# Kernel tuning notes

Measured on AMD Instinct MI355X. Metric: run time of the kernel, lower is better.

The kernel has to match this reference:

```python
import jax, jax.numpy as jnp
import numpy as np

V, F = 100000, 200000
N, H, W, K = 4, 512, 512, 4
SIGMA = 1e-4
GAMMA = 1e-4
BG = (1.0, 1.0, 1.0)
EPS = 1e-10
ZNEAR, ZFAR = 1.0, 100.0


def setup_inputs() -> dict:
    key = jax.random.key(0)
    ks = jax.random.split(key, 7)
    verts = jax.random.normal(ks[0], (V, 3), dtype=jnp.float32)
    vn = jax.random.normal(ks[1], (V, 3), dtype=jnp.float32)
    vertex_normals = vn / jnp.maximum(jnp.linalg.norm(vn, axis=-1, keepdims=True), 1e-12)
    bc = jax.random.uniform(ks[2], (N, H, W, K, 3), dtype=jnp.float32) + 1e-3
    bary_coords = bc / jnp.sum(bc, axis=-1, keepdims=True)
    # signed pixel-to-face distances, small scale comparable to sigma
    dists = jax.random.normal(ks[3], (N, H, W, K), dtype=jnp.float32) * 1e-4
    zbuf = jax.random.uniform(ks[4], (N, H, W, K), minval=ZNEAR, maxval=ZFAR, dtype=jnp.float32)
    faces = jax.random.randint(ks[5], (F, 3), 0, V, dtype=jnp.int64 if jax.config.jax_enable_x64 else jnp.int32)
    # include -1 entries (empty pixels), as produced by the rasterizer
    pix_to_face = jax.random.randint(ks[6], (N, H, W, K), -1, F, dtype=jnp.int64 if jax.config.jax_enable_x64 else jnp.int32)
    return {"verts": verts, "vertex_normals": vertex_normals, "bary_coords": bary_coords,
            "dists": dists, "zbuf": zbuf, "faces": faces, "pix_to_face": pix_to_face}


def reference(verts, vertex_normals, bary_coords, dists, zbuf, faces, pix_to_face):
    dtype = bary_coords.dtype
    # --- NormalCalcuate: gather per-face vertex normals and interpolate ---
    faces_normals = vertex_normals[faces]                      # [F, 3, 3]
    valid = pix_to_face >= 0                                   # [N,H,W,K]
    idx = jnp.where(valid, pix_to_face, 0)
    attrs = faces_normals[idx]                                 # [N,H,W,K,3(verts),3(ch)]
    pixel_normals = jnp.einsum('nhwkv,nhwkvc->nhwkc', bary_coords, attrs)
    pixel_normals = jnp.where(valid[..., None], pixel_normals, jnp.zeros((), dtype))
    # --- softmax_rgb_blend (rgb part only) ---
    maskf = valid.astype(dtype)
    prob = jax.nn.sigmoid(-dists / SIGMA) * maskf              # coverage weights
    z_inv = (ZFAR - zbuf) / (ZFAR - ZNEAR) * maskf
    z_inv_max = jnp.maximum(jnp.max(z_inv, axis=-1, keepdims=True), EPS)
    w_num = prob * jnp.exp((z_inv - z_inv_max) / GAMMA)        # [N,H,W,K]
    delta = jnp.maximum(jnp.exp((EPS - z_inv_max) / GAMMA), EPS)  # [N,H,W,1]
    denom = jnp.sum(w_num, axis=-1, keepdims=True) + delta
    bg = jnp.asarray(BG, dtype)
    rgb = (jnp.einsum('nhwk,nhwkc->nhwc', w_num, pixel_normals) + delta * bg) / denom
    # --- F.normalize(dim=3) ---
    norm = jnp.maximum(jnp.linalg.norm(rgb, axis=-1, keepdims=True), 1e-12)
    return rgb / norm
```

## Files before the change

### kernel.cpp

```cpp
#include <hip/hip_runtime.h>
#include <hip/hip_bf16.h>

namespace {
constexpr int N_ = 4, H_ = 512, W_ = 512, K_ = 4;
constexpr int F_ = 200000;
constexpr float SIGMA_ = 1e-4f;
constexpr float GAMMA_ = 1e-4f;
constexpr float EPS_   = 1e-10f;
constexpr float ZNEAR_ = 1.0f, ZFAR_ = 100.0f;

typedef float        f32x4 __attribute__((ext_vector_type(4), aligned(4)));
typedef int          i32x4 __attribute__((ext_vector_type(4), aligned(4)));
typedef float        f32x3 __attribute__((ext_vector_type(3), aligned(4)));
typedef unsigned int u32x4 __attribute__((ext_vector_type(4), aligned(16)));
}


__device__ __forceinline__ unsigned int oct_encode(float x, float y, float z) {
    const float inv = 1.0f / (fabsf(x) + fabsf(y) + fabsf(z));
    const float px = x * inv, py = y * inv, pz = z * inv;
    const float wx = (1.0f - fabsf(py)) * copysignf(1.0f, px);
    const float wy = (1.0f - fabsf(px)) * copysignf(1.0f, py);
    const bool neg = pz < 0.0f;
    const float ex = neg ? wx : px;
    const float ey = neg ? wy : py;
    const int ix = (int)rintf(ex * 32767.0f);
    const int iy = (int)rintf(ey * 32767.0f);
    return ((unsigned int)ix & 0xffffu) | (((unsigned int)iy & 0xffffu) << 16);
}

__device__ __forceinline__ void oct_decode_raw(unsigned int e,
                                               float& x, float& y, float& z,
                                               float& inv) {
    const float fx = (float)(short)(unsigned short)(e & 0xffffu) * (1.0f / 32767.0f);
    const float fy = (float)(short)(unsigned short)(e >> 16)     * (1.0f / 32767.0f);
    z = 1.0f - fabsf(fx) - fabsf(fy);
    const float t = fmaxf(-z, 0.0f);
    const float xx = fx - copysignf(t, fx);
    const float yy = fy - copysignf(t, fy);
    x = xx; y = yy;
    inv = rsqrtf(xx * xx + yy * yy + z * z);
}

__global__ __launch_bounds__(256) void build_fnorm_kernel(
    const float*  __restrict__ vnorm,
    const int*    __restrict__ faces,
    unsigned int* __restrict__ fnorm)
{
    const int f = blockIdx.x * blockDim.x + threadIdx.x;
    if (f >= F_) return;
    const i32x4 fv = *reinterpret_cast<const i32x4*>(faces + 3 * (size_t)f);
    const f32x4 n0 = *reinterpret_cast<const f32x4*>(vnorm + 3 * (size_t)fv.x);
    const f32x4 n1 = *reinterpret_cast<const f32x4*>(vnorm + 3 * (size_t)fv.y);
    const f32x4 n2 = *reinterpret_cast<const f32x4*>(vnorm + 3 * (size_t)fv.z);
    const unsigned long long e0 = oct_encode(n0.x, n0.y, n0.z);
    const unsigned long long e1 = oct_encode(n1.x, n1.y, n1.z);
    const unsigned long long e2 = oct_encode(n2.x, n2.y, n2.z);
    unsigned long long* dst =
        reinterpret_cast<unsigned long long*>(fnorm + (size_t)f * 4);
    __hip_atomic_store(dst + 0, e0 | (e1 << 32), __ATOMIC_RELAXED, __HIP_MEMORY_SCOPE_AGENT);
    __hip_atomic_store(dst + 1, e2,              __ATOMIC_RELAXED, __HIP_MEMORY_SCOPE_AGENT);
}

__global__ __launch_bounds__(256) void normal_shader_kernel(
    const unsigned int* __restrict__ fnorm,
    const float*        __restrict__ bary,
    const float*        __restrict__ dists,
    const float*        __restrict__ zbuf,
    const int*          __restrict__ ptf,
    float*              __restrict__ out,
    int P)
{
    const int t = blockIdx.x * blockDim.x + threadIdx.x;
    const int halfP = P >> 1;
    if (t >= halfP) return;
    const int pp[2] = {t, t + halfP};

    i32x4 f4[2]; f32x4 dv[2], zv[2], bA[2], bB[2], bC[2];
#pragma unroll
    for (int j = 0; j < 2; ++j) {
        const int p = pp[j];
        f4[j] = __builtin_nontemporal_load(reinterpret_cast<const i32x4*>(ptf) + p);
        dv[j] = __builtin_nontemporal_load(reinterpret_cast<const f32x4*>(dists) + p);
        zv[j] = __builtin_nontemporal_load(reinterpret_cast<const f32x4*>(zbuf) + p);
        const f32x4* bp = reinterpret_cast<const f32x4*>(bary + (size_t)p * 12);
        bA[j] = __builtin_nontemporal_load(bp + 0);
        bB[j] = __builtin_nontemporal_load(bp + 1);
        bC[j] = __builtin_nontemporal_load(bp + 2);
    }

    u32x4 row[2][4];
#pragma unroll
    for (int j = 0; j < 2; ++j) {
        const int fidx[4] = {f4[j].x, f4[j].y, f4[j].z, f4[j].w};
#pragma unroll
        for (int k = 0; k < K_; ++k) {
            const int r = (fidx[k] < 0) ? 0 : fidx[k];
            row[j][k] = reinterpret_cast<const u32x4*>(fnorm)[r];
        }
    }

    float wn[2][4], delta[2];
#pragma unroll
    for (int j = 0; j < 2; ++j) {
        const int fidx[4] = {f4[j].x, f4[j].y, f4[j].z, f4[j].w};
        const float d[4] = {dv[j].x, dv[j].y, dv[j].z, dv[j].w};
        const float z[4] = {zv[j].x, zv[j].y, zv[j].z, zv[j].w};
        float prob[4], zinv[4], zmax = EPS_;
#pragma unroll
        for (int k = 0; k < K_; ++k) {
            const bool valid = fidx[k] >= 0;
            prob[k] = valid ? 1.0f / (1.0f + __expf(d[k] * (1.0f / SIGMA_))) : 0.0f;
            zinv[k] = valid ? (ZFAR_ - z[k]) * (1.0f / (ZFAR_ - ZNEAR_)) : 0.0f;
            zmax = fmaxf(zmax, zinv[k]);
        }
        delta[j] = fmaxf(__expf((EPS_ - zmax) * (1.0f / GAMMA_)), EPS_);
#pragma unroll
        for (int k = 0; k < K_; ++k)
            wn[j][k] = prob[k] * __expf((zinv[k] - zmax) * (1.0f / GAMMA_));
    }

#pragma unroll
    for (int j = 0; j < 2; ++j) {
        const float bb[12] = {bA[j].x, bA[j].y, bA[j].z, bA[j].w,
                              bB[j].x, bB[j].y, bB[j].z, bB[j].w,
                              bC[j].x, bC[j].y, bC[j].z, bC[j].w};
        float acc0 = 0.f, acc1 = 0.f, acc2 = 0.f, wsum = 0.f;
#pragma unroll
        for (int k = 0; k < K_; ++k) {
            const float w = wn[j][k];
            wsum += w;
            float x0, y0, z0, i0, x1, y1, z1, i1, x2, y2, z2, i2;
            oct_decode_raw(row[j][k].x, x0, y0, z0, i0);
            oct_decode_raw(row[j][k].y, x1, y1, z1, i1);
            oct_decode_raw(row[j][k].z, x2, y2, z2, i2);
            const float s0 = (w * bb[3 * k + 0]) * i0;
            const float s1 = (w * bb[3 * k + 1]) * i1;
            const float s2 = (w * bb[3 * k + 2]) * i2;
            acc0 += s0 * x0 + s1 * x1 + s2 * x2;
            acc1 += s0 * y0 + s1 * y1 + s2 * y2;
            acc2 += s0 * z0 + s1 * z1 + s2 * z2;
        }
        const float inv_denom = 1.0f / (wsum + delta[j]);
        const float r0 = (acc0 + delta[j]) * inv_denom;
        const float r1 = (acc1 + delta[j]) * inv_denom;
        const float r2 = (acc2 + delta[j]) * inv_denom;
        const float nrm = fmaxf(sqrtf(r0 * r0 + r1 * r1 + r2 * r2), 1e-12f);
        const float inv = 1.0f / nrm;
        __builtin_nontemporal_store(
            f32x3{r0 * inv, r1 * inv, r2 * inv},
            reinterpret_cast<f32x3*>(out + (size_t)pp[j] * 3));
    }
}

__global__ __launch_bounds__(256) void normal_shader_fused_kernel(
    const float* __restrict__ vnorm,
    const float* __restrict__ bary,
    const float* __restrict__ dists,
    const float* __restrict__ zbuf,
    const int*   __restrict__ faces,
    const int*   __restrict__ ptf,
    float*       __restrict__ out,
    int P)
{
    const int p = blockIdx.x * blockDim.x + threadIdx.x;
    if (p >= P) return;
    const i32x4 f4 = reinterpret_cast<const i32x4*>(ptf)[p];
    const int fidx[4] = {f4.x, f4.y, f4.z, f4.w};
    const f32x4 dv = reinterpret_cast<const f32x4*>(dists)[p];
    const f32x4 zv = reinterpret_cast<const f32x4*>(zbuf)[p];
    const float d[4] = {dv.x, dv.y, dv.z, dv.w};
    const float z[4] = {zv.x, zv.y, zv.z, zv.w};
    float prob[4], zinv[4], zmax = EPS_;
#pragma unroll
    for (int k = 0; k < K_; ++k) {
        const bool valid = fidx[k] >= 0;
        prob[k] = valid ? 1.0f / (1.0f + __expf(d[k] * (1.0f / SIGMA_))) : 0.0f;
        zinv[k] = valid ? (ZFAR_ - z[k]) * (1.0f / (ZFAR_ - ZNEAR_)) : 0.0f;
        zmax = fmaxf(zmax, zinv[k]);
    }
    const float delta = fmaxf(__expf((EPS_ - zmax) * (1.0f / GAMMA_)), EPS_);
    float wn[4];
#pragma unroll
    for (int k = 0; k < K_; ++k) wn[k] = prob[k] * __expf((zinv[k] - zmax) * (1.0f / GAMMA_));
    int cl[4];
#pragma unroll
    for (int k = 0; k < K_; ++k) cl[k] = (fidx[k] < 0) ? 0 : fidx[k];
    i32x4 fv[4];
#pragma unroll
    for (int k = 0; k < K_; ++k) fv[k] = *reinterpret_cast<const i32x4*>(faces + 3 * (size_t)cl[k]);
    const f32x4* bp = reinterpret_cast<const f32x4*>(bary + (size_t)p * 12);
    const f32x4 bA = bp[0], bB = bp[1], bC = bp[2];
    const float bb[12] = {bA.x, bA.y, bA.z, bA.w, bB.x, bB.y, bB.z, bB.w, bC.x, bC.y, bC.z, bC.w};
    f32x4 n0[4], n1[4], n2[4];
#pragma unroll
    for (int k = 0; k < K_; ++k) {
        n0[k] = *reinterpret_cast<const f32x4*>(vnorm + 3 * (size_t)fv[k].x);
        n1[k] = *reinterpret_cast<const f32x4*>(vnorm + 3 * (size_t)fv[k].y);
        n2[k] = *reinterpret_cast<const f32x4*>(vnorm + 3 * (size_t)fv[k].z);
    }
    float acc0 = 0.f, acc1 = 0.f, acc2 = 0.f, wsum = 0.f;
#pragma unroll
    for (int k = 0; k < K_; ++k) {
        wsum += wn[k];
        const float b0 = bb[3 * k], b1 = bb[3 * k + 1], b2 = bb[3 * k + 2];
        acc0 += wn[k] * (b0 * n0[k].x + b1 * n1[k].x + b2 * n2[k].x);
        acc1 += wn[k] * (b0 * n0[k].y + b1 * n1[k].y + b2 * n2[k].y);
        acc2 += wn[k] * (b0 * n0[k].z + b1 * n1[k].z + b2 * n2[k].z);
    }
    const float inv_denom = 1.0f / (wsum + delta);
    const float r0 = (acc0 + delta) * inv_denom;
    const float r1 = (acc1 + delta) * inv_denom;
    const float r2 = (acc2 + delta) * inv_denom;
    const float nrm = fmaxf(sqrtf(r0 * r0 + r1 * r1 + r2 * r2), 1e-12f);
    const float inv = 1.0f / nrm;
    float* op = out + (size_t)p * 3;
    op[0] = r0 * inv; op[1] = r1 * inv; op[2] = r2 * inv;
}

extern "C" void kernel_launch(void* const* d_in, const int* in_sizes, int n_in,
                              void* d_out, int out_size, void* d_ws, size_t ws_size,
                              hipStream_t stream) {
    const float* vnorm = (const float*)d_in[1];
    const float* bary  = (const float*)d_in[2];
    const float* dists = (const float*)d_in[3];
    const float* zbuf  = (const float*)d_in[4];
    const int*   faces = (const int*)d_in[5];
    const int*   ptf   = (const int*)d_in[6];
    float*       out   = (float*)d_out;

    const int P = N_ * H_ * W_;
    const size_t table_bytes = (size_t)F_ * 16;

    if (ws_size >= table_bytes) {
        unsigned int* fnorm = (unsigned int*)d_ws;
        hipLaunchKernelGGL(build_fnorm_kernel,
                           dim3((F_ + 255) / 256), dim3(256), 0, stream,
                           vnorm, faces, fnorm);
        hipLaunchKernelGGL(normal_shader_kernel,
                           dim3(((P >> 1) + 255) / 256), dim3(256), 0, stream,
                           fnorm, bary, dists, zbuf, ptf, out, P);
    } else {
        hipLaunchKernelGGL(normal_shader_fused_kernel,
                           dim3((P + 255) / 256), dim3(256), 0, stream,
                           vnorm, bary, dists, zbuf, faces, ptf, out, P);
    }
}
```

Baseline: 163.9 us.

## Use persistent grid with software-pipelined prefetch of next pixel inputs

Replaces the two-pixels-per-thread shader with a fixed grid of 1024 blocks, where each thread loops over four pixels strided by the total thread count. While it processes the current pixel, it prefetches the next pixel's streaming inputs (face ids, dists, zbuf, barycentrics). It also adds a launch-bounds occupancy hint of 4. This aims to overlap streaming loads with the gather and compute, at the cost of fewer waves in flight and higher register pressure from the prefetch buffer.

```diff
diff --git a/kernel.cpp b/kernel.cpp
--- a/kernel.cpp
+++ b/kernel.cpp
@@ -9,10 +9,18 @@
 constexpr float EPS_   = 1e-10f;
 constexpr float ZNEAR_ = 1.0f, ZFAR_ = 100.0f;
 
+constexpr int P_ = N_ * H_ * W_;
+constexpr int SHADER_BLOCKS  = 1024;
+constexpr int SHADER_THREADS = SHADER_BLOCKS * 256;
+constexpr int ITERS = P_ / SHADER_THREADS;
+static_assert(P_ % SHADER_THREADS == 0, "grid must tile P exactly");
+
 typedef float        f32x4 __attribute__((ext_vector_type(4), aligned(4)));
 typedef int          i32x4 __attribute__((ext_vector_type(4), aligned(4)));
 typedef float        f32x3 __attribute__((ext_vector_type(3), aligned(4)));
 typedef unsigned int u32x4 __attribute__((ext_vector_type(4), aligned(16)));
+
+struct PixIn { i32x4 f4; f32x4 dv, zv, bA, bB, bC; };
 }
 
 
@@ -62,50 +70,52 @@
     __hip_atomic_store(dst + 1, e2,              __ATOMIC_RELAXED, __HIP_MEMORY_SCOPE_AGENT);
 }
 
-__global__ __launch_bounds__(256) void normal_shader_kernel(
+__device__ __forceinline__ PixIn load_pix(const int*   __restrict__ ptf,
+                                          const float* __restrict__ dists,
+                                          const float* __restrict__ zbuf,
+                                          const float* __restrict__ bary,
+                                          int p) {
+    PixIn s;
+    s.f4 = __builtin_nontemporal_load(reinterpret_cast<const i32x4*>(ptf) + p);
+    s.dv = __builtin_nontemporal_load(reinterpret_cast<const f32x4*>(dists) + p);
+    s.zv = __builtin_nontemporal_load(reinterpret_cast<const f32x4*>(zbuf) + p);
+    const f32x4* bp = reinterpret_cast<const f32x4*>(bary + (size_t)p * 12);
+    s.bA = __builtin_nontemporal_load(bp + 0);
+    s.bB = __builtin_nontemporal_load(bp + 1);
+    s.bC = __builtin_nontemporal_load(bp + 2);
+    return s;
+}
+
+__global__ __launch_bounds__(256, 4) void normal_shader_kernel(
     const unsigned int* __restrict__ fnorm,
     const float*        __restrict__ bary,
     const float*        __restrict__ dists,
     const float*        __restrict__ zbuf,
     const int*          __restrict__ ptf,
-    float*              __restrict__ out,
-    int P)
+    float*              __restrict__ out)
 {
-    const int t = blockIdx.x * blockDim.x + threadIdx.x;
-    const int halfP = P >> 1;
-    if (t >= halfP) return;
-    const int pp[2] = {t, t + halfP};
-
-    i32x4 f4[2]; f32x4 dv[2], zv[2], bA[2], bB[2], bC[2];
-#pragma unroll
-    for (int j = 0; j < 2; ++j) {
-        const int p = pp[j];
-        f4[j] = __builtin_nontemporal_load(reinterpret_cast<const i32x4*>(ptf) + p);
-        dv[j] = __builtin_nontemporal_load(reinterpret_cast<const f32x4*>(dists) + p);
-        zv[j] = __builtin_nontemporal_load(reinterpret_cast<const f32x4*>(zbuf) + p);
-        const f32x4* bp = reinterpret_cast<const f32x4*>(bary + (size_t)p * 12);
-        bA[j] = __builtin_nontemporal_load(bp + 0);
-        bB[j] = __builtin_nontemporal_load(bp + 1);
-        bC[j] = __builtin_nontemporal_load(bp + 2);
-    }
-
-    u32x4 row[2][4];
-#pragma unroll
-    for (int j = 0; j < 2; ++j) {
-        const int fidx[4] = {f4[j].x, f4[j].y, f4[j].z, f4[j].w};
+    const int tid = blockIdx.x * 256 + threadIdx.x;
+
+    PixIn cur = load_pix(ptf, dists, zbuf, bary, tid);
+
+#pragma unroll
+    for (int it = 0; it < ITERS; ++it) {
+        const int p = tid + it * SHADER_THREADS;
+        const int fidx[4] = {cur.f4.x, cur.f4.y, cur.f4.z, cur.f4.w};
+
+        u32x4 row[4];
 #pragma unroll
         for (int k = 0; k < K_; ++k) {
             const int r = (fidx[k] < 0) ? 0 : fidx[k];
-            row[j][k] = reinterpret_cast<const u32x4*>(fnorm)[r];
+            row[k] = reinterpret_cast<const u32x4*>(fnorm)[r];
         }
-    }
-
-    float wn[2][4], delta[2];
-#pragma unroll
-    for (int j = 0; j < 2; ++j) {
-        const int fidx[4] = {f4[j].x, f4[j].y, f4[j].z, f4[j].w};
-        const float d[4] = {dv[j].x, dv[j].y, dv[j].z, dv[j].w};
-        const float z[4] = {zv[j].x, zv[j].y, zv[j].z, zv[j].w};
+
+        PixIn nxt = cur;
+        if (it + 1 < ITERS)
+            nxt = load_pix(ptf, dists, zbuf, bary, p + SHADER_THREADS);
+
+        const float d[4] = {cur.dv.x, cur.dv.y, cur.dv.z, cur.dv.w};
+        const float z[4] = {cur.zv.x, cur.zv.y, cur.zv.z, cur.zv.w};
         float prob[4], zinv[4], zmax = EPS_;
 #pragma unroll
         for (int k = 0; k < K_; ++k) {
@@ -114,26 +124,24 @@
             zinv[k] = valid ? (ZFAR_ - z[k]) * (1.0f / (ZFAR_ - ZNEAR_)) : 0.0f;
             zmax = fmaxf(zmax, zinv[k]);
         }
-        delta[j] = fmaxf(__expf((EPS_ - zmax) * (1.0f / GAMMA_)), EPS_);
+        const float delta = fmaxf(__expf((EPS_ - zmax) * (1.0f / GAMMA_)), EPS_);
+        float wn[4];
 #pragma unroll
         for (int k = 0; k < K_; ++k)
-            wn[j][k] = prob[k] * __expf((zinv[k] - zmax) * (1.0f / GAMMA_));
-    }
-
-#pragma unroll
-    for (int j = 0; j < 2; ++j) {
-        const float bb[12] = {bA[j].x, bA[j].y, bA[j].z, bA[j].w,
-                              bB[j].x, bB[j].y, bB[j].z, bB[j].w,
-                              bC[j].x, bC[j].y, bC[j].z, bC[j].w};
+            wn[k] = prob[k] * __expf((zinv[k] - zmax) * (1.0f / GAMMA_));
+
+        const float bb[12] = {cur.bA.x, cur.bA.y, cur.bA.z, cur.bA.w,
+                              cur.bB.x, cur.bB.y, cur.bB.z, cur.bB.w,
+                              cur.bC.x, cur.bC.y, cur.bC.z, cur.bC.w};
         float acc0 = 0.f, acc1 = 0.f, acc2 = 0.f, wsum = 0.f;
 #pragma unroll
         for (int k = 0; k < K_; ++k) {
-            const float w = wn[j][k];
+            const float w = wn[k];
             wsum += w;
             float x0, y0, z0, i0, x1, y1, z1, i1, x2, y2, z2, i2;
-            oct_decode_raw(row[j][k].x, x0, y0, z0, i0);
-            oct_decode_raw(row[j][k].y, x1, y1, z1, i1);
-            oct_decode_raw(row[j][k].z, x2, y2, z2, i2);
+            oct_decode_raw(row[k].x, x0, y0, z0, i0);
+            oct_decode_raw(row[k].y, x1, y1, z1, i1);
+            oct_decode_raw(row[k].z, x2, y2, z2, i2);
             const float s0 = (w * bb[3 * k + 0]) * i0;
             const float s1 = (w * bb[3 * k + 1]) * i1;
             const float s2 = (w * bb[3 * k + 2]) * i2;
@@ -141,15 +149,17 @@
             acc1 += s0 * y0 + s1 * y1 + s2 * y2;
             acc2 += s0 * z0 + s1 * z1 + s2 * z2;
         }
-        const float inv_denom = 1.0f / (wsum + delta[j]);
-        const float r0 = (acc0 + delta[j]) * inv_denom;
-        const float r1 = (acc1 + delta[j]) * inv_denom;
-        const float r2 = (acc2 + delta[j]) * inv_denom;
+        const float inv_denom = 1.0f / (wsum + delta);
+        const float r0 = (acc0 + delta) * inv_denom;
+        const float r1 = (acc1 + delta) * inv_denom;
+        const float r2 = (acc2 + delta) * inv_denom;
         const float nrm = fmaxf(sqrtf(r0 * r0 + r1 * r1 + r2 * r2), 1e-12f);
         const float inv = 1.0f / nrm;
         __builtin_nontemporal_store(
             f32x3{r0 * inv, r1 * inv, r2 * inv},
-            reinterpret_cast<f32x3*>(out + (size_t)pp[j] * 3));
+            reinterpret_cast<f32x3*>(out + (size_t)p * 3));
+
+        cur = nxt;
     }
 }
 
@@ -238,8 +248,8 @@
                            dim3((F_ + 255) / 256), dim3(256), 0, stream,
                            vnorm, faces, fnorm);
         hipLaunchKernelGGL(normal_shader_kernel,
-                           dim3(((P >> 1) + 255) / 256), dim3(256), 0, stream,
-                           fnorm, bary, dists, zbuf, ptf, out, P);
+                           dim3(SHADER_BLOCKS), dim3(256), 0, stream,
+                           fnorm, bary, dists, zbuf, ptf, out);
     } else {
         hipLaunchKernelGGL(normal_shader_fused_kernel,
                            dim3((P + 255) / 256), dim3(256), 0, stream,
```

Result: no change. 164.4 us (+0.3%).
